# Kernel optimization log

Hardware: AMD Instinct MI355X
Metric: run time of the kernel (lower is better)

Reference implementation:

```python
import jax, jax.numpy as jnp
import numpy as np

NUM_HEADS = 16

def setup_inputs() -> dict:
    key = jax.random.key(0)
    k1, k2, k3 = jax.random.split(key, 3)
    D = 1024
    return {
        "hidden_states": jax.random.normal(k1, (2, 2048, D), dtype=jnp.float32),
        "c_attn_w": jax.random.normal(k2, (D, 3 * D), dtype=jnp.float32) * 0.02,
        "c_attn_b": jnp.zeros((3 * D,), dtype=jnp.float32),
        "c_proj_w": jax.random.normal(k3, (D, D), dtype=jnp.float32) * 0.02,
        "c_proj_b": jnp.zeros((D,), dtype=jnp.float32),
    }

def reference(hidden_states, c_attn_w, c_attn_b, c_proj_w, c_proj_b):
    B, S, D = hidden_states.shape
    H = NUM_HEADS
    hd = D // H
    # Conv1D: x @ W + b, then split into q, k, v
    qkv = hidden_states @ c_attn_w + c_attn_b  # [B, S, 3D]
    q, k, v = jnp.split(qkv, 3, axis=-1)
    q = q.reshape(B, S, H, hd).transpose(0, 2, 1, 3)  # [B, H, S, hd]
    k = k.reshape(B, S, H, hd).transpose(0, 2, 1, 3)
    v = v.reshape(B, S, H, hd).transpose(0, 2, 1, 3)
    # scaled QK^T
    scores = jnp.einsum("bhqd,bhkd->bhqk", q, k) / jnp.asarray(hd ** 0.5, q.dtype)
    # causal mask (tril), masked positions set to dtype min per original code
    causal = jnp.tril(jnp.ones((S, S), dtype=bool))
    mask_value = jnp.finfo(scores.dtype).min
    scores = jnp.where(causal[None, None], scores, mask_value)
    attn = jax.nn.softmax(scores, axis=-1)
    out = jnp.einsum("bhqk,bhkd->bhqd", attn, v)  # [B, H, S, hd]
    out = out.transpose(0, 2, 1, 3).reshape(B, S, D)
    out = out @ c_proj_w + c_proj_b
    return out
```

## Files before the change

### kernel.cpp

```cpp
#include <hip/hip_runtime.h>
#include <hip/hip_bf16.h>
#include <math.h>

#define B_ 2
#define S_ 2048
#define D_ 1024
#define H_ 16
#define HD 64
#define M_ (B_ * S_)
#define N_QKV (3 * D_)

typedef short short8 __attribute__((ext_vector_type(8)));
typedef float floatx4 __attribute__((ext_vector_type(4)));

static __device__ __forceinline__ unsigned short f2bf(float x) {
    __hip_bfloat16 h = __float2bfloat16(x);
    unsigned short u;
    __builtin_memcpy(&u, &h, sizeof(u));
    return u;
}
static __device__ __forceinline__ float bf2f(unsigned short b) {
    union { unsigned u; float f; } v; v.u = ((unsigned)b) << 16;
    return v.f;
}
static __device__ __forceinline__ void split2(float x, unsigned short& h, unsigned short& l) {
    h = f2bf(x);
    l = f2bf(x - bf2f(h));
}

static __device__ __forceinline__ void dma16(const void* g, void* l) {
    __builtin_amdgcn_global_load_lds(
        (const __attribute__((address_space(1))) unsigned int*)g,
        (__attribute__((address_space(3))) unsigned int*)l,
        16, 0, 0);
}

__global__ __launch_bounds__(256) void prep_all(
    const float* __restrict__ hs,
    const float* __restrict__ attn_w,
    const float* __restrict__ proj_w,
    unsigned short* __restrict__ Ahi, unsigned short* __restrict__ Alo,
    unsigned short* __restrict__ WqThi, unsigned short* __restrict__ WqTlo,
    unsigned short* __restrict__ WpThi, unsigned short* __restrict__ WpTlo)
{
    __shared__ float Ws[64][68];
    const int bid = blockIdx.x;
    const int t   = threadIdx.x;

    if (bid < 2048) {
        const size_t i = ((size_t)bid * 256 + t) * 8;
        float4 a = *(const float4*)(hs + i);
        float4 b = *(const float4*)(hs + i + 4);
        float xs[8] = {a.x, a.y, a.z, a.w, b.x, b.y, b.z, b.w};
        short8 h, l;
#pragma unroll
        for (int e = 0; e < 8; e++) {
            unsigned short hh, ll;
            split2(xs[e], hh, ll);
            h[e] = (short)hh; l[e] = (short)ll;
        }
        *(short8*)&Ahi[i] = h;
        *(short8*)&Alo[i] = l;
        return;
    }

    const float* W; unsigned short *Thi, *Tlo; int N, n0, k0;
    if (bid < 2816) {
        const int s = bid - 2048;
        W = attn_w; Thi = WqThi; Tlo = WqTlo; N = N_QKV;
        n0 = (s % 48) * 64; k0 = (s / 48) * 64;
    } else {
        const int s = bid - 2816;
        W = proj_w; Thi = WpThi; Tlo = WpTlo; N = D_;
        n0 = (s % 16) * 64; k0 = (s / 16) * 64;
    }
    {
        const int kl = t >> 4, nl = (t & 15) * 4;
        const float* src = W + (size_t)(k0 + kl) * N + n0 + nl;
#pragma unroll
        for (int g = 0; g < 4; g++)
            *(float4*)&Ws[kl + g * 16][nl] = *(const float4*)(src + (size_t)g * 16 * N);
    }
    __syncthreads();
    {
        const int nl = t >> 2, ks = (t & 3) * 16;
        short8 h0, h1, l0, l1;
#pragma unroll
        for (int j = 0; j < 8; j++) {
            unsigned short hh, ll;
            split2(Ws[ks + j][nl], hh, ll);
            h0[j] = (short)hh; l0[j] = (short)ll;
        }
#pragma unroll
        for (int j = 0; j < 8; j++) {
            unsigned short hh, ll;
            split2(Ws[ks + 8 + j][nl], hh, ll);
            h1[j] = (short)hh; l1[j] = (short)ll;
        }
        unsigned short* dh = Thi + (size_t)(n0 + nl) * D_ + k0 + ks;
        unsigned short* dl = Tlo + (size_t)(n0 + nl) * D_ + k0 + ks;
        *(short8*)dh = h0; *(short8*)(dh + 8) = h1;
        *(short8*)dl = l0; *(short8*)(dl + 8) = l1;
    }
}

__global__ __launch_bounds__(256) void gemm_qkv(
    const unsigned short* __restrict__ Ahi, const unsigned short* __restrict__ Alo,
    const unsigned short* __restrict__ BThi, const unsigned short* __restrict__ BTlo,
    const float* __restrict__ bias,
    unsigned short* __restrict__ Qhi, unsigned short* __restrict__ Qlo,
    unsigned short* __restrict__ Khi, unsigned short* __restrict__ Klo,
    unsigned short* __restrict__ vThi, unsigned short* __restrict__ vTlo)
{
    __shared__ unsigned short sAh[128 * 32], sAl[128 * 32];
    __shared__ unsigned short sBh[128 * 32], sBl[128 * 32];

    const int t    = threadIdx.x;
    const int m0   = blockIdx.y * 128, n0 = blockIdx.x * 128;
    const int lane = t & 63, wave = t >> 6;
    const int lm   = lane & 15, quad = lane >> 4;
    const int wm   = (wave >> 1) * 64, wn = (wave & 1) * 64;

    const int lrow = lane >> 2, lcol = (lane & 3) * 8;
    const unsigned short* gAh = Ahi + (size_t)(m0 + wave * 32 + lrow) * D_ + lcol;
    const unsigned short* gAl = Alo + (size_t)(m0 + wave * 32 + lrow) * D_ + lcol;
    const unsigned short* gBh = BThi + (size_t)(n0 + wave * 32 + lrow) * D_ + lcol;
    const unsigned short* gBl = BTlo + (size_t)(n0 + wave * 32 + lrow) * D_ + lcol;
    const int ldst = wave * 1024 + lane * 8;

    floatx4 acc[4][4];
#pragma unroll
    for (int i = 0; i < 4; i++)
#pragma unroll
        for (int j = 0; j < 4; j++)
#pragma unroll
            for (int r = 0; r < 4; r++) acc[i][j][r] = 0.f;

    for (int k0 = 0; k0 < D_; k0 += 32) {
        __syncthreads();
        dma16(gAh + k0, &sAh[ldst]);
        dma16(gAh + (size_t)16 * D_ + k0, &sAh[ldst + 512]);
        dma16(gAl + k0, &sAl[ldst]);
        dma16(gAl + (size_t)16 * D_ + k0, &sAl[ldst + 512]);
        dma16(gBh + k0, &sBh[ldst]);
        dma16(gBh + (size_t)16 * D_ + k0, &sBh[ldst + 512]);
        dma16(gBl + k0, &sBl[ldst]);
        dma16(gBl + (size_t)16 * D_ + k0, &sBl[ldst + 512]);
        __syncthreads();

        short8 bhf[4], blf[4];
#pragma unroll
        for (int nb = 0; nb < 4; nb++) {
            const int r = wn + nb * 16 + lm;
            bhf[nb] = *(const short8*)&sBh[r * 32 + quad * 8];
            blf[nb] = *(const short8*)&sBl[r * 32 + quad * 8];
        }
#pragma unroll
        for (int mb = 0; mb < 4; mb++) {
            const int r = wm + mb * 16 + lm;
            short8 ah = *(const short8*)&sAh[r * 32 + quad * 8];
            short8 al = *(const short8*)&sAl[r * 32 + quad * 8];
#pragma unroll
            for (int nb = 0; nb < 4; nb++) {
                acc[mb][nb] = __builtin_amdgcn_mfma_f32_16x16x32_bf16(ah, bhf[nb], acc[mb][nb], 0, 0, 0);
                acc[mb][nb] = __builtin_amdgcn_mfma_f32_16x16x32_bf16(al, bhf[nb], acc[mb][nb], 0, 0, 0);
                acc[mb][nb] = __builtin_amdgcn_mfma_f32_16x16x32_bf16(ah, blf[nb], acc[mb][nb], 0, 0, 0);
            }
        }
    }

    const int nmode = n0 >> 10;
    if (nmode == 0) {
#pragma unroll
        for (int nb = 0; nb < 4; nb++) {
            const int c = n0 + wn + nb * 16 + lm;
            const float bv = bias[c];
#pragma unroll
            for (int mb = 0; mb < 4; mb++) {
                const int rowb = m0 + wm + mb * 16 + quad * 4;
#pragma unroll
                for (int r = 0; r < 4; r++) {
                    unsigned short hh, ll;
                    split2((acc[mb][nb][r] + bv) * 0.125f, hh, ll);
                    Qhi[(size_t)(rowb + r) * D_ + c] = hh;
                    Qlo[(size_t)(rowb + r) * D_ + c] = ll;
                }
            }
        }
    } else if (nmode == 1) {
#pragma unroll
        for (int nb = 0; nb < 4; nb++) {
            const int c = n0 + wn + nb * 16 + lm;
            const float bv = bias[c];
            const int cq = c - 1024;
#pragma unroll
            for (int mb = 0; mb < 4; mb++) {
                const int rowb = m0 + wm + mb * 16 + quad * 4;
#pragma unroll
                for (int r = 0; r < 4; r++) {
                    unsigned short hh, ll;
                    split2(acc[mb][nb][r] + bv, hh, ll);
                    Khi[(size_t)(rowb + r) * D_ + cq] = hh;
                    Klo[(size_t)(rowb + r) * D_ + cq] = ll;
                }
            }
        }
    } else {
#pragma unroll
        for (int nb = 0; nb < 4; nb++) {
            const int c = n0 + wn + nb * 16 + lm;
            const float bv = bias[c];
            const int cq = c - 2048;
            const int hh_ = cq >> 6, dd = cq & 63;
#pragma unroll
            for (int mb = 0; mb < 4; mb++) {
                const int rowb = m0 + wm + mb * 16 + quad * 4;
                const int bb = rowb >> 11, ss = rowb & 2047;
                unsigned short hv[4], lv[4];
#pragma unroll
                for (int r = 0; r < 4; r++)
                    split2(acc[mb][nb][r] + bv, hv[r], lv[r]);
                const size_t idx = ((size_t)((bb * 16 + hh_) * 64 + dd)) * S_ + ss;
                *(uint2*)&vThi[idx] = make_uint2((unsigned)hv[0] | ((unsigned)hv[1] << 16),
                                                 (unsigned)hv[2] | ((unsigned)hv[3] << 16));
                *(uint2*)&vTlo[idx] = make_uint2((unsigned)lv[0] | ((unsigned)lv[1] << 16),
                                                 (unsigned)lv[2] | ((unsigned)lv[3] << 16));
            }
        }
    }
}

__global__ __launch_bounds__(256) void gemm_out(
    const unsigned short* __restrict__ Ahi, const unsigned short* __restrict__ Alo,
    const unsigned short* __restrict__ BThi, const unsigned short* __restrict__ BTlo,
    const float* __restrict__ bias, float* __restrict__ C)
{
    __shared__ unsigned short sAh[64 * 32], sAl[64 * 32];
    __shared__ unsigned short sBh[64 * 32], sBl[64 * 32];

    const int t   = threadIdx.x;
    const int lid = blockIdx.x;
    const int swz = (lid & 7) * 128 + (lid >> 3);
    const int bx  = swz & 15, by = swz >> 4;
    const int m0  = by * 64, n0 = bx * 64;
    const int lane = t & 63, wave = t >> 6;
    const int lm   = lane & 15, quad = lane >> 4;

    const int lrow = lane >> 2, lcol = (lane & 3) * 8;
    const unsigned short* gAh = Ahi + (size_t)(m0 + wave * 16 + lrow) * D_ + lcol;
    const unsigned short* gAl = Alo + (size_t)(m0 + wave * 16 + lrow) * D_ + lcol;
    const unsigned short* gBh = BThi + (size_t)(n0 + wave * 16 + lrow) * D_ + lcol;
    const unsigned short* gBl = BTlo + (size_t)(n0 + wave * 16 + lrow) * D_ + lcol;
    unsigned short* lAh = sAh + wave * 512 + lane * 8;
    unsigned short* lAl = sAl + wave * 512 + lane * 8;
    unsigned short* lBh = sBh + wave * 512 + lane * 8;
    unsigned short* lBl = sBl + wave * 512 + lane * 8;

    floatx4 acc[4];
#pragma unroll
    for (int j = 0; j < 4; j++)
#pragma unroll
        for (int r = 0; r < 4; r++) acc[j][r] = 0.f;

    for (int k0 = 0; k0 < D_; k0 += 32) {
        __syncthreads();
        dma16(gAh + k0, lAh);
        dma16(gAl + k0, lAl);
        dma16(gBh + k0, lBh);
        dma16(gBl + k0, lBl);
        __syncthreads();

        short8 ah = *(const short8*)&sAh[(wave * 16 + lm) * 32 + quad * 8];
        short8 al = *(const short8*)&sAl[(wave * 16 + lm) * 32 + quad * 8];
#pragma unroll
        for (int nb = 0; nb < 4; nb++) {
            short8 bh = *(const short8*)&sBh[(nb * 16 + lm) * 32 + quad * 8];
            short8 bl = *(const short8*)&sBl[(nb * 16 + lm) * 32 + quad * 8];
            acc[nb] = __builtin_amdgcn_mfma_f32_16x16x32_bf16(ah, bh, acc[nb], 0, 0, 0);
            acc[nb] = __builtin_amdgcn_mfma_f32_16x16x32_bf16(al, bh, acc[nb], 0, 0, 0);
            acc[nb] = __builtin_amdgcn_mfma_f32_16x16x32_bf16(ah, bl, acc[nb], 0, 0, 0);
        }
    }

#pragma unroll
    for (int nb = 0; nb < 4; nb++) {
        const int col = n0 + nb * 16 + lm;
        const float bv = bias[col];
#pragma unroll
        for (int r = 0; r < 4; r++) {
            const int row = m0 + wave * 16 + quad * 4 + r;
            C[(size_t)row * D_ + col] = acc[nb][r] + bv;
        }
    }
}

#define PSP 72

__global__ __launch_bounds__(512, 4) void flash_attn_mfma(
    unsigned short* QAhi, unsigned short* QAlo,
    const unsigned short* __restrict__ Khi, const unsigned short* __restrict__ Klo,
    const unsigned short* __restrict__ vThi, const unsigned short* __restrict__ vTlo)
{
    __shared__ unsigned short KhS[64 * 64], KlS[64 * 64];
    __shared__ unsigned short VhS[64 * 64], VlS[64 * 64];
    __shared__ unsigned short PhS[128 * PSP], PlS[128 * PSP];

    const int t    = threadIdx.x;
    const int lid  = blockIdx.x + 16 * blockIdx.y;
    const int bh   = (lid & 7) * 4 + ((lid >> 3) & 3);
    const int pj   = lid >> 5;
    const int b    = bh >> 4, h = bh & 15;
    const int lane = t & 63, w = t >> 6;
    const int lm   = lane & 15, quad = lane >> 4;

    const int qt = (bh & 1) ? (15 - pj) : pj;
    const int q0 = qt * 128;
    const int ntiles = 2 * qt + 2;
    const int wdiag = (q0 >> 6) + (w >> 2);

    const int r0  = t >> 3;
    const int seg = (t & 7) ^ (r0 & 7);
    const unsigned short* gKh = Khi + (size_t)(b * S_ + r0) * D_ + h * HD + 8 * seg;
    const unsigned short* gKl = Klo + (size_t)(b * S_ + r0) * D_ + h * HD + 8 * seg;
    const unsigned short* gVh = vThi + ((size_t)((b * 16 + h) * 64 + r0)) * S_ + 8 * seg;
    const unsigned short* gVl = vTlo + ((size_t)((b * 16 + h) * 64 + r0)) * S_ + 8 * seg;
    const int ld0 = t * 8;
    const int swzr = (lm & 7) << 3;

    short8 qh[2], ql[2];
    {
        const size_t qoff = (size_t)(b * S_ + q0 + 16 * w + lm) * D_ + h * HD + quad * 8;
        qh[0] = *(const short8*)&QAhi[qoff];
        qh[1] = *(const short8*)&QAhi[qoff + 32];
        ql[0] = *(const short8*)&QAlo[qoff];
        ql[1] = *(const short8*)&QAlo[qoff + 32];
    }

    float lsum[4] = {0.f, 0.f, 0.f, 0.f};
    floatx4 o[4];
#pragma unroll
    for (int nb = 0; nb < 4; nb++)
#pragma unroll
        for (int r = 0; r < 4; r++) o[nb][r] = 0.f;

    for (int kt = 0; kt < ntiles; kt++) {
        __syncthreads();
        {
            const size_t ko = (size_t)(kt * 64) * D_;
            const int vo = kt * 64;
            dma16(gKh + ko, &KhS[ld0]);
            dma16(gKl + ko, &KlS[ld0]);
            dma16(gVh + vo, &VhS[ld0]);
            dma16(gVl + vo, &VlS[ld0]);
        }
        __syncthreads();

        if (kt <= wdiag) {
            floatx4 sa[4];
#pragma unroll
            for (int nb = 0; nb < 4; nb++)
#pragma unroll
                for (int r = 0; r < 4; r++) sa[nb][r] = 0.f;
            __builtin_amdgcn_s_setprio(1);
#pragma unroll
            for (int s = 0; s < 2; s++) {
#pragma unroll
                for (int nb = 0; nb < 4; nb++) {
                    const int ka = (nb * 16 + lm) * 64 + ((s * 32 + quad * 8) ^ swzr);
                    short8 kh = *(const short8*)&KhS[ka];
                    short8 kl = *(const short8*)&KlS[ka];
                    sa[nb] = __builtin_amdgcn_mfma_f32_16x16x32_bf16(qh[s], kh, sa[nb], 0, 0, 0);
                    sa[nb] = __builtin_amdgcn_mfma_f32_16x16x32_bf16(ql[s], kh, sa[nb], 0, 0, 0);
                    sa[nb] = __builtin_amdgcn_mfma_f32_16x16x32_bf16(qh[s], kl, sa[nb], 0, 0, 0);
                }
            }
            __builtin_amdgcn_s_setprio(0);

            const bool diag = (kt == wdiag);
            const int kbase = kt * 64;
#pragma unroll
            for (int r = 0; r < 4; r++) {
                const int qabs = q0 + 16 * w + 4 * quad + r;
                const int rloc = 16 * w + 4 * quad + r;
#pragma unroll
                for (int nb = 0; nb < 4; nb++) {
                    float p = __expf(sa[nb][r]);
                    if (diag && (kbase + 16 * nb + lm > qabs)) p = 0.f;
                    lsum[r] += p;
                    unsigned short hh, ll;
                    split2(p, hh, ll);
                    PhS[rloc * PSP + 16 * nb + lm] = hh;
                    PlS[rloc * PSP + 16 * nb + lm] = ll;
                }
            }

            __builtin_amdgcn_s_setprio(1);
#pragma unroll
            for (int ks = 0; ks < 2; ks++) {
                short8 pf = *(const short8*)&PhS[(16 * w + lm) * PSP + ks * 32 + quad * 8];
                short8 pg = *(const short8*)&PlS[(16 * w + lm) * PSP + ks * 32 + quad * 8];
#pragma unroll
                for (int nb = 0; nb < 4; nb++) {
                    const int va = (nb * 16 + lm) * 64 + ((ks * 32 + quad * 8) ^ swzr);
                    short8 vhf = *(const short8*)&VhS[va];
                    short8 vlf = *(const short8*)&VlS[va];
                    o[nb] = __builtin_amdgcn_mfma_f32_16x16x32_bf16(pf, vhf, o[nb], 0, 0, 0);
                    o[nb] = __builtin_amdgcn_mfma_f32_16x16x32_bf16(pg, vhf, o[nb], 0, 0, 0);
                    o[nb] = __builtin_amdgcn_mfma_f32_16x16x32_bf16(pf, vlf, o[nb], 0, 0, 0);
                }
            }
            __builtin_amdgcn_s_setprio(0);
        }
    }

#pragma unroll
    for (int r = 0; r < 4; r++) {
        float l = lsum[r];
        l += __shfl_xor(l, 1);
        l += __shfl_xor(l, 2);
        l += __shfl_xor(l, 4);
        l += __shfl_xor(l, 8);
        const float inv = 1.f / l;
        const size_t rowoff =
            (size_t)(b * S_ + q0 + 16 * w + 4 * quad + r) * D_ + h * HD + lm;
#pragma unroll
        for (int nb = 0; nb < 4; nb++) {
            unsigned short hh, ll;
            split2(o[nb][r] * inv, hh, ll);
            QAhi[rowoff + 16 * nb] = hh;
            QAlo[rowoff + 16 * nb] = ll;
        }
    }
}

extern "C" void kernel_launch(void* const* d_in, const int* in_sizes, int n_in,
                              void* d_out, int out_size, void* d_ws, size_t ws_size,
                              hipStream_t stream)
{
    const float* hs     = (const float*)d_in[0];
    const float* attn_w = (const float*)d_in[1];
    const float* attn_b = (const float*)d_in[2];
    const float* proj_w = (const float*)d_in[3];
    const float* proj_b = (const float*)d_in[4];
    float* outp = (float*)d_out;

    const size_t QE = (size_t)M_ * D_;
    const size_t WQ = (size_t)D_ * N_QKV;
    unsigned short* Qhi   = (unsigned short*)d_ws;
    unsigned short* Qlo   = Qhi + QE;
    unsigned short* Khi   = Qlo + QE;
    unsigned short* Klo   = Khi + QE;
    unsigned short* vThi  = Klo + QE;
    unsigned short* vTlo  = vThi + QE;
    unsigned short* WqThi = vTlo + QE;
    unsigned short* WqTlo = WqThi + WQ;
    unsigned short* WpThi = WqTlo + WQ;
    unsigned short* WpTlo = WpThi + (size_t)D_ * D_;
    unsigned short* Ahi   = WpTlo + (size_t)D_ * D_;
    unsigned short* Alo   = Ahi + QE;

    dim3 blk(256);
    prep_all<<<dim3(3072), blk, 0, stream>>>(
        hs, attn_w, proj_w, Ahi, Alo, WqThi, WqTlo, WpThi, WpTlo);
    gemm_qkv<<<dim3(N_QKV / 128, M_ / 128), blk, 0, stream>>>(
        Ahi, Alo, WqThi, WqTlo, attn_b, Qhi, Qlo, Khi, Klo, vThi, vTlo);
    flash_attn_mfma<<<dim3(16, B_ * H_), dim3(512), 0, stream>>>(
        Qhi, Qlo, Khi, Klo, vThi, vTlo);
    gemm_out<<<dim3(1024), blk, 0, stream>>>(
        Qhi, Qlo, WpThi, WpTlo, proj_b, outp);
}
```

Before: 301.9 us.

## Double K-step in output GEMM with swizzled LDS and use exp2 in attention

The output projection GEMM now loads 64-wide K tiles per barrier pair instead of 32, halving the number of syncthreads rounds. It also XOR-swizzles the LDS layout to avoid bank conflicts on the 64-element rows. Separately, Q is prescaled by log2(e)/8 so the attention softmax can use exp2f instead of __expf. The larger tiles double LDS use in the GEMM, and the softmax change folds a constant into Q, which slightly changes rounding.

```diff
diff --git a/kernel.cpp b/kernel.cpp
--- a/kernel.cpp
+++ b/kernel.cpp
@@ -9,6 +9,7 @@
 #define HD 64
 #define M_ (B_ * S_)
 #define N_QKV (3 * D_)
+#define LOG2E_8 0.18033688011112042f
 
 typedef short short8 __attribute__((ext_vector_type(8)));
 typedef float floatx4 __attribute__((ext_vector_type(4)));
@@ -181,7 +182,7 @@
 #pragma unroll
                 for (int r = 0; r < 4; r++) {
                     unsigned short hh, ll;
-                    split2((acc[mb][nb][r] + bv) * 0.125f, hh, ll);
+                    split2((acc[mb][nb][r] + bv) * LOG2E_8, hh, ll);
                     Qhi[(size_t)(rowb + r) * D_ + c] = hh;
                     Qlo[(size_t)(rowb + r) * D_ + c] = ll;
                 }
@@ -235,8 +236,8 @@
     const unsigned short* __restrict__ BThi, const unsigned short* __restrict__ BTlo,
     const float* __restrict__ bias, float* __restrict__ C)
 {
-    __shared__ unsigned short sAh[64 * 32], sAl[64 * 32];
-    __shared__ unsigned short sBh[64 * 32], sBl[64 * 32];
+    __shared__ unsigned short sAh[64 * 64], sAl[64 * 64];
+    __shared__ unsigned short sBh[64 * 64], sBl[64 * 64];
 
     const int t   = threadIdx.x;
     const int lid = blockIdx.x;
@@ -246,15 +247,14 @@
     const int lane = t & 63, wave = t >> 6;
     const int lm   = lane & 15, quad = lane >> 4;
 
-    const int lrow = lane >> 2, lcol = (lane & 3) * 8;
-    const unsigned short* gAh = Ahi + (size_t)(m0 + wave * 16 + lrow) * D_ + lcol;
-    const unsigned short* gAl = Alo + (size_t)(m0 + wave * 16 + lrow) * D_ + lcol;
-    const unsigned short* gBh = BThi + (size_t)(n0 + wave * 16 + lrow) * D_ + lcol;
-    const unsigned short* gBl = BTlo + (size_t)(n0 + wave * 16 + lrow) * D_ + lcol;
-    unsigned short* lAh = sAh + wave * 512 + lane * 8;
-    unsigned short* lAl = sAl + wave * 512 + lane * 8;
-    unsigned short* lBh = sBh + wave * 512 + lane * 8;
-    unsigned short* lBl = sBl + wave * 512 + lane * 8;
+    const int r0   = t >> 3;
+    const int gseg = (t & 7) ^ (r0 & 7);
+    const unsigned short* gAh = Ahi + (size_t)(m0 + r0) * D_ + gseg * 8;
+    const unsigned short* gAl = Alo + (size_t)(m0 + r0) * D_ + gseg * 8;
+    const unsigned short* gBh = BThi + (size_t)(n0 + r0) * D_ + gseg * 8;
+    const unsigned short* gBl = BTlo + (size_t)(n0 + r0) * D_ + gseg * 8;
+    const int ld0  = t * 8;
+    const int swzr = lm & 7;
 
     floatx4 acc[4];
 #pragma unroll
@@ -262,23 +262,32 @@
 #pragma unroll
         for (int r = 0; r < 4; r++) acc[j][r] = 0.f;
 
-    for (int k0 = 0; k0 < D_; k0 += 32) {
-        __syncthreads();
-        dma16(gAh + k0, lAh);
-        dma16(gAl + k0, lAl);
-        dma16(gBh + k0, lBh);
-        dma16(gBl + k0, lBl);
-        __syncthreads();
-
-        short8 ah = *(const short8*)&sAh[(wave * 16 + lm) * 32 + quad * 8];
-        short8 al = *(const short8*)&sAl[(wave * 16 + lm) * 32 + quad * 8];
-#pragma unroll
-        for (int nb = 0; nb < 4; nb++) {
-            short8 bh = *(const short8*)&sBh[(nb * 16 + lm) * 32 + quad * 8];
-            short8 bl = *(const short8*)&sBl[(nb * 16 + lm) * 32 + quad * 8];
-            acc[nb] = __builtin_amdgcn_mfma_f32_16x16x32_bf16(ah, bh, acc[nb], 0, 0, 0);
-            acc[nb] = __builtin_amdgcn_mfma_f32_16x16x32_bf16(al, bh, acc[nb], 0, 0, 0);
-            acc[nb] = __builtin_amdgcn_mfma_f32_16x16x32_bf16(ah, bl, acc[nb], 0, 0, 0);
+    for (int k0 = 0; k0 < D_; k0 += 64) {
+        __syncthreads();
+        dma16(gAh + k0, &sAh[ld0]);
+        dma16(gAh + (size_t)32 * D_ + k0, &sAh[ld0 + 2048]);
+        dma16(gAl + k0, &sAl[ld0]);
+        dma16(gAl + (size_t)32 * D_ + k0, &sAl[ld0 + 2048]);
+        dma16(gBh + k0, &sBh[ld0]);
+        dma16(gBh + (size_t)32 * D_ + k0, &sBh[ld0 + 2048]);
+        dma16(gBl + k0, &sBl[ld0]);
+        dma16(gBl + (size_t)32 * D_ + k0, &sBl[ld0 + 2048]);
+        __syncthreads();
+
+#pragma unroll
+        for (int ks = 0; ks < 2; ks++) {
+            const int arow = (wave * 16 + lm) * 64 + (((ks * 4 + quad) ^ swzr) * 8);
+            short8 ah = *(const short8*)&sAh[arow];
+            short8 al = *(const short8*)&sAl[arow];
+#pragma unroll
+            for (int nb = 0; nb < 4; nb++) {
+                const int brow = (nb * 16 + lm) * 64 + (((ks * 4 + quad) ^ swzr) * 8);
+                short8 bh = *(const short8*)&sBh[brow];
+                short8 bl = *(const short8*)&sBl[brow];
+                acc[nb] = __builtin_amdgcn_mfma_f32_16x16x32_bf16(ah, bh, acc[nb], 0, 0, 0);
+                acc[nb] = __builtin_amdgcn_mfma_f32_16x16x32_bf16(al, bh, acc[nb], 0, 0, 0);
+                acc[nb] = __builtin_amdgcn_mfma_f32_16x16x32_bf16(ah, bl, acc[nb], 0, 0, 0);
+            }
         }
     }
 
@@ -384,7 +393,7 @@
                 const int rloc = 16 * w + 4 * quad + r;
 #pragma unroll
                 for (int nb = 0; nb < 4; nb++) {
-                    float p = __expf(sa[nb][r]);
+                    float p = exp2f(sa[nb][r]);
                     if (diag && (kbase + 16 * nb + lm > qabs)) p = 0.f;
                     lsum[r] += p;
                     unsigned short hh, ll;
```

New measurement: 299.1 us. About the same (-0.9%).
